# Kernel tuning notes

Measured on AMD Instinct MI355X. Metric: run time of the kernel, lower is better.

## Reference

```python
import jax, jax.numpy as jnp
import numpy as np

B, D_IN, D_OUT, N_DISJOINT = 4096, 256, 256, 64


def setup_inputs() -> dict:
    key = jax.random.key(0)
    k_x, k_sel, k_w, k_b = jax.random.split(key, 4)
    x = jax.random.normal(k_x, (B, D_IN), dtype=jnp.float32)
    sel_idx = jax.random.randint(k_sel, (B,), 0, N_DISJOINT)
    one_hot_selector = jax.nn.one_hot(sel_idx, N_DISJOINT, dtype=jnp.float32)
    # torch nn.Linear default init: U(-1/sqrt(fan_in), 1/sqrt(fan_in)), fan_in = num_disjoint
    bound = 1.0 / np.sqrt(N_DISJOINT)
    # W[d] is the [in, out] weight matrix for disjoint block d
    W = jax.random.uniform(k_w, (N_DISJOINT, D_IN, D_OUT), dtype=jnp.float32, minval=-bound, maxval=bound)
    Bw = jax.random.uniform(k_b, (N_DISJOINT, D_OUT), dtype=jnp.float32, minval=-bound, maxval=bound)
    return {"x": x, "one_hot_selector": one_hot_selector, "W": W, "Bw": Bw}


def reference(x, one_hot_selector, W, Bw):
    # Same math as: w = (selector @ weights.T).view(B, in, out); h = einsum('bij,bi->bj', w, x)
    # Reordered contraction avoids the [B, in, out] intermediate:
    v = jnp.einsum('bi,dio->bdo', x, W)          # [B, D, out]
    h = jnp.einsum('bd,bdo->bo', one_hot_selector, v)  # [B, out]
    bias = one_hot_selector @ Bw                  # [B, out]
    return h + bias
```

## Files before the change

kernel.cpp:

```cpp
#include <hip/hip_runtime.h>


#define NBLK 64
#define BCAP 1024
#define CPAD 16

typedef __attribute__((ext_vector_type(8))) short bf16x8;
typedef __attribute__((ext_vector_type(4))) float f32x4;

__device__ __forceinline__ unsigned short f2bf(float f) {
    unsigned u = __float_as_uint(f);
    u += 0x7FFFu + ((u >> 16) & 1u);
    return (unsigned short)(u >> 16);
}

__global__ __launch_bounds__(256) void dd_bucketize(
    const float* __restrict__ onehot,
    int* __restrict__ counts,
    int* __restrict__ buckets)
{
    __shared__ int rowd[256];
    __shared__ int lhist[NBLK];
    __shared__ int lbase[NBLK];
    const int t = threadIdx.x;
    const int w = t >> 6;
    const int lane = t & 63;
    if (t < NBLK) lhist[t] = 0;

    const int row0 = blockIdx.x * 256 + w * 64;
#pragma unroll 8
    for (int i = 0; i < 64; ++i) {
        const float v = onehot[(size_t)(row0 + i) * NBLK + lane];
        const unsigned long long m = __ballot(v > 0.5f);
        const int d = (int)__ffsll(m) - 1;
        if (lane == 0) rowd[w * 64 + i] = d;
    }
    __syncthreads();

    const int d = rowd[t];
    const int slot = atomicAdd(&lhist[d], 1);
    __syncthreads();
    if (t < NBLK) lbase[t] = atomicAdd(&counts[t * CPAD], lhist[t]);
    __syncthreads();
    buckets[d * BCAP + lbase[d] + slot] = blockIdx.x * 256 + t;
}

__global__ __launch_bounds__(256, 2) void dd_compute(
    const float* __restrict__ x,
    const float* __restrict__ W,
    const float* __restrict__ Bw,
    const int* __restrict__ counts,
    const int* __restrict__ buckets,
    float* __restrict__ out)
{
    __shared__ unsigned short xbf[32][264];
    __shared__ int lrid[32];

    const int t    = threadIdx.x;
    const int lane = t & 63;
    const int w    = t >> 6;
    const int d    = blockIdx.x & 63;
    const int q    = blockIdx.x >> 6;
    const int rt   = q >> 2;
    const int ct   = q & 3;
    const int cw   = ct * 64 + w * 16;
    const int m    = lane & 15;
    const int qd   = lane >> 4;

    const int cnt = counts[d * CPAD];
    const float* Wd = W + ((size_t)d << 16);
    const float bias = Bw[d * 256 + cw + m];

    for (int base = rt * 32; base < cnt; base += 64) {
        {
            const int row = t >> 3;
            const int kc  = (t & 7) * 32;
            const int idx = base + row;
            const int r = buckets[d * BCAP + (idx < cnt ? idx : cnt - 1)];
            if ((t & 7) == 0) lrid[row] = r;
            const float* xp = x + ((size_t)r << 8) + kc;
#pragma unroll
            for (int i = 0; i < 8; ++i) {
                const float4 v = *(const float4*)(xp + i * 4);
                ushort4 b;
                b.x = f2bf(v.x); b.y = f2bf(v.y); b.z = f2bf(v.z); b.w = f2bf(v.w);
                *(ushort4*)&xbf[row][kc + i * 4] = b;
            }
        }
        __syncthreads();

        bf16x8 bfrag[8];
#pragma unroll
        for (int kb = 0; kb < 8; ++kb) {
            const float* wp = Wd + (size_t)(kb * 32 + qd * 8) * 256 + (cw + m);
#pragma unroll
            for (int j = 0; j < 8; ++j)
                bfrag[kb][j] = (short)f2bf(wp[j * 256]);
        }

        f32x4 acc0 = {bias, bias, bias, bias};
        f32x4 acc1 = {bias, bias, bias, bias};
        const int koff = qd * 8;
#pragma unroll
        for (int kb = 0; kb < 8; ++kb) {
            bf16x8 a = *(const bf16x8*)&xbf[m][kb * 32 + koff];
            acc0 = __builtin_amdgcn_mfma_f32_16x16x32_bf16(a, bfrag[kb], acc0, 0, 0, 0);
        }
#pragma unroll
        for (int kb = 0; kb < 8; ++kb) {
            bf16x8 a = *(const bf16x8*)&xbf[16 + m][kb * 32 + koff];
            acc1 = __builtin_amdgcn_mfma_f32_16x16x32_bf16(a, bfrag[kb], acc1, 0, 0, 0);
        }

#pragma unroll
        for (int reg = 0; reg < 4; ++reg) {
            const int rl0 = qd * 4 + reg;
            if (base + rl0 < cnt)
                out[(size_t)lrid[rl0] * 256 + cw + m] = acc0[reg];
            const int rl1 = 16 + qd * 4 + reg;
            if (base + rl1 < cnt)
                out[(size_t)lrid[rl1] * 256 + cw + m] = acc1[reg];
        }
        __syncthreads();
    }
}

extern "C" void kernel_launch(void* const* d_in, const int* in_sizes, int n_in,
                              void* d_out, int out_size, void* d_ws, size_t ws_size,
                              hipStream_t stream) {
    const float* x      = (const float*)d_in[0];
    const float* onehot = (const float*)d_in[1];
    const float* W      = (const float*)d_in[2];
    const float* Bw     = (const float*)d_in[3];
    float* out = (float*)d_out;

    int* counts  = (int*)d_ws;
    int* buckets = (int*)((char*)d_ws + NBLK * CPAD * 4);

    hipMemsetAsync(counts, 0, NBLK * CPAD * sizeof(int), stream);
    dd_bucketize<<<16, 256, 0, stream>>>(onehot, counts, buckets);
    dd_compute<<<512, 256, 0, stream>>>(x, W, Bw, counts, buckets, out);
}
```

Baseline: 97.65 us.

## Pre-swizzle W to bf16 MFMA fragments, hoist weight loads, widen bucketize grid

```diff
diff --git a/kernel.cpp b/kernel.cpp
--- a/kernel.cpp
+++ b/kernel.cpp
@@ -14,12 +14,35 @@
     return (unsigned short)(u >> 16);
 }
 
+__global__ __launch_bounds__(256) void dd_swizzle(
+    const float* __restrict__ W,
+    unsigned short* __restrict__ Wb,
+    int* __restrict__ counts)
+{
+    if (blockIdx.x == 0 && threadIdx.x < NBLK) counts[threadIdx.x * CPAD] = 0;
+    const int t = threadIdx.x, lane = t & 63, w = t >> 6;
+    const int d    = blockIdx.x & 63;
+    const int task = (blockIdx.x >> 6) * 4 + w;
+    const int c16  = task >> 3;
+    const int kb   = task & 7;
+    const int m = lane & 15, qd = lane >> 4;
+
+    const float* wp = W + ((size_t)d << 16)
+                        + (size_t)(kb * 32 + qd * 8) * 256 + c16 * 16 + m;
+    bf16x8 frag;
+#pragma unroll
+    for (int j = 0; j < 8; ++j) frag[j] = (short)f2bf(wp[j * 256]);
+
+    unsigned short* dst = Wb + ((size_t)((d * 16 + c16) * 8 + kb) * 64 + lane) * 8;
+    *(bf16x8*)dst = frag;
+}
+
 __global__ __launch_bounds__(256) void dd_bucketize(
     const float* __restrict__ onehot,
     int* __restrict__ counts,
     int* __restrict__ buckets)
 {
-    __shared__ int rowd[256];
+    __shared__ int rowd[128];
     __shared__ int lhist[NBLK];
     __shared__ int lbase[NBLK];
     const int t = threadIdx.x;
@@ -27,27 +50,30 @@
     const int lane = t & 63;
     if (t < NBLK) lhist[t] = 0;
 
-    const int row0 = blockIdx.x * 256 + w * 64;
+    const int row0 = blockIdx.x * 128 + w * 32;
 #pragma unroll 8
-    for (int i = 0; i < 64; ++i) {
+    for (int i = 0; i < 32; ++i) {
         const float v = onehot[(size_t)(row0 + i) * NBLK + lane];
-        const unsigned long long m = __ballot(v > 0.5f);
-        const int d = (int)__ffsll(m) - 1;
-        if (lane == 0) rowd[w * 64 + i] = d;
+        const unsigned long long mm = __ballot(v > 0.5f);
+        const int d = (int)__ffsll(mm) - 1;
+        if (lane == 0) rowd[w * 32 + i] = d;
     }
     __syncthreads();
 
-    const int d = rowd[t];
-    const int slot = atomicAdd(&lhist[d], 1);
+    int d = 0, slot = 0;
+    if (t < 128) {
+        d = rowd[t];
+        slot = atomicAdd(&lhist[d], 1);
+    }
     __syncthreads();
     if (t < NBLK) lbase[t] = atomicAdd(&counts[t * CPAD], lhist[t]);
     __syncthreads();
-    buckets[d * BCAP + lbase[d] + slot] = blockIdx.x * 256 + t;
+    if (t < 128) buckets[d * BCAP + lbase[d] + slot] = blockIdx.x * 128 + t;
 }
 
-__global__ __launch_bounds__(256, 2) void dd_compute(
+__global__ __launch_bounds__(256) void dd_compute(
     const float* __restrict__ x,
-    const float* __restrict__ W,
+    const unsigned short* __restrict__ Wb,
     const float* __restrict__ Bw,
     const int* __restrict__ counts,
     const int* __restrict__ buckets,
@@ -68,35 +94,29 @@
     const int qd   = lane >> 4;
 
     const int cnt = counts[d * CPAD];
-    const float* Wd = W + ((size_t)d << 16);
     const float bias = Bw[d * 256 + cw + m];
 
+    bf16x8 bfrag[8];
+    const unsigned short* wbase =
+        Wb + ((size_t)(d * 16 + ct * 4 + w) * 8) * 512 + (size_t)lane * 8;
+#pragma unroll
+    for (int kb = 0; kb < 8; ++kb)
+        bfrag[kb] = *(const bf16x8*)(wbase + (size_t)kb * 512);
+
     for (int base = rt * 32; base < cnt; base += 64) {
-        {
-            const int row = t >> 3;
-            const int kc  = (t & 7) * 32;
-            const int idx = base + row;
-            const int r = buckets[d * BCAP + (idx < cnt ? idx : cnt - 1)];
-            if ((t & 7) == 0) lrid[row] = r;
-            const float* xp = x + ((size_t)r << 8) + kc;
+        if (t < 32) lrid[t] = buckets[d * BCAP + (base + t < cnt ? base + t : cnt - 1)];
+        __syncthreads();
+
 #pragma unroll
-            for (int i = 0; i < 8; ++i) {
-                const float4 v = *(const float4*)(xp + i * 4);
-                ushort4 b;
-                b.x = f2bf(v.x); b.y = f2bf(v.y); b.z = f2bf(v.z); b.w = f2bf(v.w);
-                *(ushort4*)&xbf[row][kc + i * 4] = b;
-            }
+        for (int p = 0; p < 8; ++p) {
+            const int row = p * 4 + w;
+            const int r = lrid[row];
+            const float4 v = ((const float4*)(x + ((size_t)r << 8)))[lane];
+            ushort4 b;
+            b.x = f2bf(v.x); b.y = f2bf(v.y); b.z = f2bf(v.z); b.w = f2bf(v.w);
+            *(ushort4*)&xbf[row][lane * 4] = b;
         }
         __syncthreads();
-
-        bf16x8 bfrag[8];
-#pragma unroll
-        for (int kb = 0; kb < 8; ++kb) {
-            const float* wp = Wd + (size_t)(kb * 32 + qd * 8) * 256 + (cw + m);
-#pragma unroll
-            for (int j = 0; j < 8; ++j)
-                bfrag[kb][j] = (short)f2bf(wp[j * 256]);
-        }
 
         f32x4 acc0 = {bias, bias, bias, bias};
         f32x4 acc1 = {bias, bias, bias, bias};
@@ -136,8 +156,9 @@
 
     int* counts  = (int*)d_ws;
     int* buckets = (int*)((char*)d_ws + NBLK * CPAD * 4);
+    unsigned short* Wb = (unsigned short*)((char*)d_ws + NBLK * CPAD * 4 + NBLK * BCAP * 4);
 
-    hipMemsetAsync(counts, 0, NBLK * CPAD * sizeof(int), stream);
-    dd_bucketize<<<16, 256, 0, stream>>>(onehot, counts, buckets);
-    dd_compute<<<512, 256, 0, stream>>>(x, W, Bw, counts, buckets, out);
+    dd_swizzle<<<2048, 256, 0, stream>>>(W, Wb, counts);
+    dd_bucketize<<<32, 256, 0, stream>>>(onehot, counts, buckets);
+    dd_compute<<<512, 256, 0, stream>>>(x, Wb, Bw, counts, buckets, out);
 }
```

Result: faster. 92.50 us (-5.3%).

## Pre-convert x to bf16 in prep kernel and load MFMA operands directly from global

Applied to the files above, without the earlier changes.

```diff
diff --git a/kernel.cpp b/kernel.cpp
--- a/kernel.cpp
+++ b/kernel.cpp
@@ -14,12 +14,14 @@
     return (unsigned short)(u >> 16);
 }
 
-__global__ __launch_bounds__(256) void dd_bucketize(
+__global__ __launch_bounds__(256) void dd_prep(
+    const float* __restrict__ x,
     const float* __restrict__ onehot,
     int* __restrict__ counts,
-    int* __restrict__ buckets)
+    int* __restrict__ buckets,
+    unsigned short* __restrict__ xb)
 {
-    __shared__ int rowd[256];
+    __shared__ int rowd[32];
     __shared__ int lhist[NBLK];
     __shared__ int lbase[NBLK];
     const int t = threadIdx.x;
@@ -27,101 +29,107 @@
     const int lane = t & 63;
     if (t < NBLK) lhist[t] = 0;
 
-    const int row0 = blockIdx.x * 256 + w * 64;
-#pragma unroll 8
-    for (int i = 0; i < 64; ++i) {
-        const float v = onehot[(size_t)(row0 + i) * NBLK + lane];
-        const unsigned long long m = __ballot(v > 0.5f);
-        const int d = (int)__ffsll(m) - 1;
-        if (lane == 0) rowd[w * 64 + i] = d;
+    const int row0 = blockIdx.x * 32;
+#pragma unroll
+    for (int i = 0; i < 8; ++i) {
+        const int row = row0 + w * 8 + i;
+        const float v = onehot[(size_t)row * NBLK + lane];
+        const unsigned long long mm = __ballot(v > 0.5f);
+        const int d = (int)__ffsll(mm) - 1;
+        if (lane == 0) rowd[w * 8 + i] = d;
+    }
+#pragma unroll
+    for (int i = 0; i < 8; ++i) {
+        const int row = row0 + w * 8 + i;
+        const float4 v = ((const float4*)(x + ((size_t)row << 8)))[lane];
+        ushort4 b;
+        b.x = f2bf(v.x); b.y = f2bf(v.y); b.z = f2bf(v.z); b.w = f2bf(v.w);
+        *(ushort4*)(xb + ((size_t)row << 8) + lane * 4) = b;
     }
     __syncthreads();
 
-    const int d = rowd[t];
-    const int slot = atomicAdd(&lhist[d], 1);
+    int d = 0, slot = 0;
+    if (t < 32) {
+        d = rowd[t];
+        slot = atomicAdd(&lhist[d], 1);
+    }
     __syncthreads();
-    if (t < NBLK) lbase[t] = atomicAdd(&counts[t * CPAD], lhist[t]);
+    if (t < NBLK && lhist[t] > 0)
+        lbase[t] = atomicAdd(&counts[t * CPAD], lhist[t]);
     __syncthreads();
-    buckets[d * BCAP + lbase[d] + slot] = blockIdx.x * 256 + t;
+    if (t < 32) buckets[d * BCAP + lbase[d] + slot] = row0 + t;
 }
 
-__global__ __launch_bounds__(256, 2) void dd_compute(
-    const float* __restrict__ x,
+__global__ __launch_bounds__(256) void dd_compute(
+    const unsigned short* __restrict__ xb,
     const float* __restrict__ W,
     const float* __restrict__ Bw,
     const int* __restrict__ counts,
     const int* __restrict__ buckets,
     float* __restrict__ out)
 {
-    __shared__ unsigned short xbf[32][264];
-    __shared__ int lrid[32];
-
     const int t    = threadIdx.x;
     const int lane = t & 63;
     const int w    = t >> 6;
     const int d    = blockIdx.x & 63;
-    const int q    = blockIdx.x >> 6;
-    const int rt   = q >> 2;
-    const int ct   = q & 3;
+    const int task = blockIdx.x >> 6;
+    const int rt   = task >> 2;
+    const int ct   = task & 3;
     const int cw   = ct * 64 + w * 16;
     const int m    = lane & 15;
     const int qd   = lane >> 4;
 
     const int cnt = counts[d * CPAD];
-    const float* Wd = W + ((size_t)d << 16);
+    if (rt * 32 >= cnt) return;
+
+    const float* wb = W + ((size_t)d << 16) + (size_t)(qd * 8) * 256 + (cw + m);
+    bf16x8 bfrag[8];
+#pragma unroll
+    for (int kb = 0; kb < 8; ++kb) {
+        const float* wp = wb + (size_t)(kb * 32) * 256;
+#pragma unroll
+        for (int j = 0; j < 8; ++j)
+            bfrag[kb][j] = (short)f2bf(wp[j * 256]);
+    }
+
     const float bias = Bw[d * 256 + cw + m];
+    const int* bkt = buckets + d * BCAP;
 
-    for (int base = rt * 32; base < cnt; base += 64) {
-        {
-            const int row = t >> 3;
-            const int kc  = (t & 7) * 32;
-            const int idx = base + row;
-            const int r = buckets[d * BCAP + (idx < cnt ? idx : cnt - 1)];
-            if ((t & 7) == 0) lrid[row] = r;
-            const float* xp = x + ((size_t)r << 8) + kc;
-#pragma unroll
-            for (int i = 0; i < 8; ++i) {
-                const float4 v = *(const float4*)(xp + i * 4);
-                ushort4 b;
-                b.x = f2bf(v.x); b.y = f2bf(v.y); b.z = f2bf(v.z); b.w = f2bf(v.w);
-                *(ushort4*)&xbf[row][kc + i * 4] = b;
-            }
-        }
-        __syncthreads();
+    for (int base = rt * 32; base < cnt; base += 128) {
+        const int i0 = base + m;
+        const int i1 = base + 16 + m;
+        const int r0 = bkt[i0 < cnt ? i0 : cnt - 1];
+        const int r1 = bkt[i1 < cnt ? i1 : cnt - 1];
 
-        bf16x8 bfrag[8];
-#pragma unroll
-        for (int kb = 0; kb < 8; ++kb) {
-            const float* wp = Wd + (size_t)(kb * 32 + qd * 8) * 256 + (cw + m);
-#pragma unroll
-            for (int j = 0; j < 8; ++j)
-                bfrag[kb][j] = (short)f2bf(wp[j * 256]);
-        }
+        const unsigned short* xp0 = xb + ((size_t)r0 << 8) + qd * 8;
+        const unsigned short* xp1 = xb + ((size_t)r1 << 8) + qd * 8;
 
         f32x4 acc0 = {bias, bias, bias, bias};
         f32x4 acc1 = {bias, bias, bias, bias};
-        const int koff = qd * 8;
 #pragma unroll
         for (int kb = 0; kb < 8; ++kb) {
-            bf16x8 a = *(const bf16x8*)&xbf[m][kb * 32 + koff];
-            acc0 = __builtin_amdgcn_mfma_f32_16x16x32_bf16(a, bfrag[kb], acc0, 0, 0, 0);
+            bf16x8 a0 = *(const bf16x8*)(xp0 + kb * 32);
+            acc0 = __builtin_amdgcn_mfma_f32_16x16x32_bf16(a0, bfrag[kb], acc0, 0, 0, 0);
         }
 #pragma unroll
         for (int kb = 0; kb < 8; ++kb) {
-            bf16x8 a = *(const bf16x8*)&xbf[16 + m][kb * 32 + koff];
-            acc1 = __builtin_amdgcn_mfma_f32_16x16x32_bf16(a, bfrag[kb], acc1, 0, 0, 0);
+            bf16x8 a1 = *(const bf16x8*)(xp1 + kb * 32);
+            acc1 = __builtin_amdgcn_mfma_f32_16x16x32_bf16(a1, bfrag[kb], acc1, 0, 0, 0);
         }
 
 #pragma unroll
         for (int reg = 0; reg < 4; ++reg) {
-            const int rl0 = qd * 4 + reg;
-            if (base + rl0 < cnt)
-                out[(size_t)lrid[rl0] * 256 + cw + m] = acc0[reg];
-            const int rl1 = 16 + qd * 4 + reg;
-            if (base + rl1 < cnt)
-                out[(size_t)lrid[rl1] * 256 + cw + m] = acc1[reg];
+            const int rl0 = base + qd * 4 + reg;
+            if (rl0 < cnt) {
+                const int rr = bkt[rl0];
+                out[((size_t)rr << 8) + cw + m] = acc0[reg];
+            }
+            const int rl1 = base + 16 + qd * 4 + reg;
+            if (rl1 < cnt) {
+                const int rr = bkt[rl1];
+                out[((size_t)rr << 8) + cw + m] = acc1[reg];
+            }
         }
-        __syncthreads();
     }
 }
 
@@ -136,8 +144,9 @@
 
     int* counts  = (int*)d_ws;
     int* buckets = (int*)((char*)d_ws + NBLK * CPAD * 4);
+    unsigned short* xb = (unsigned short*)((char*)d_ws + NBLK * CPAD * 4 + NBLK * BCAP * 4);
 
     hipMemsetAsync(counts, 0, NBLK * CPAD * sizeof(int), stream);
-    dd_bucketize<<<16, 256, 0, stream>>>(onehot, counts, buckets);
-    dd_compute<<<512, 256, 0, stream>>>(x, W, Bw, counts, buckets, out);
+    dd_prep<<<128, 256, 0, stream>>>(x, onehot, counts, buckets, xb);
+    dd_compute<<<1024, 256, 0, stream>>>(xb, W, Bw, counts, buckets, out);
 }
```

Measured after the change: 85.83 us (median of 2 runs). -12.1%, faster.
